# Performance work log

Hardware: AMD Instinct MI355X
Metric: run time of the kernel (lower is better)

Reference implementation:

```python
import jax, jax.numpy as jnp
import numpy as np

B, N, D = 2048, 64, 256  # batch, n_linears, n_in == n_out
N_RECURS = 3             # loop runs n_recurs + 1 = 4 times


def _make_masks():
    # per-group active block sizes in [128, 256], mimicking _init_masks
    n_act = np.minimum(128 + 32 * (np.arange(N) % 5), D)  # [N]
    col = np.arange(D)
    active = col[None, :] < n_act[:, None]                 # [N, D]
    w_mask = (active[:, :, None] & active[:, None, :]).astype(np.float32)  # [N, D, D]
    b_mask = active.astype(np.float32)                     # [N, D]
    return jnp.asarray(w_mask), jnp.asarray(b_mask)


def setup_inputs() -> dict:
    key = jax.random.key(0)
    k1, k2, k3 = jax.random.split(key, 3)
    x = jax.random.normal(k1, (B, N, D), dtype=jnp.float32)
    # kaiming_uniform-like scale for fan_in = D
    bound = 1.0 / np.sqrt(D)
    weights = jax.random.uniform(k2, (N, D, D), dtype=jnp.float32, minval=-bound, maxval=bound)
    biases = jax.random.uniform(k3, (N, D), dtype=jnp.float32, minval=-bound, maxval=bound)
    weight_mask, bias_mask = _make_masks()
    return {"x": x, "weights": weights, "biases": biases,
            "weight_mask": weight_mask, "bias_mask": bias_mask}


def reference(x, weights, biases, weight_mask, bias_mask):
    # Mask is static across recurrence steps; torch code recomputes it each
    # step but the values are identical, so hoist (same math).
    w = weights * weight_mask          # [N, D, D]
    b = (biases * bias_mask)[None]     # [1, N, D]
    for _ in range(N_RECURS + 1):
        # grouped small GEMM: x[b,n,i] @ w[n,j,i]^T -> [b,n,j]
        x = x + jax.nn.relu(jnp.einsum('bni,nji->bnj', x, w) + b)
    return x
```

## Files before the change

kernel.cpp:

```cpp
#include <hip/hip_runtime.h>
#include <hip/hip_bf16.h>
#include <cstdint>
#include <cstddef>

#define B_TOT   2048
#define N_LIN   64
#define D_DIM   256
#define NSTEPS  4
#define BT      64

typedef __attribute__((ext_vector_type(8))) short short8;
typedef __attribute__((ext_vector_type(4))) float f32x4;

__device__ __forceinline__ void split2(float f, unsigned short& h, unsigned short& l) {
    unsigned u = __float_as_uint(f);
    unsigned r = u + 0x7FFFu + ((u >> 16) & 1u);
    h = (unsigned short)(r >> 16);
    float hf = __uint_as_float(r & 0xFFFF0000u);
    float rem = f - hf;
    unsigned u2 = __float_as_uint(rem);
    unsigned r2 = u2 + 0x7FFFu + ((u2 >> 16) & 1u);
    l = (unsigned short)(r2 >> 16);
}

__device__ __forceinline__ float bf16_to_f(unsigned short s) {
    return __uint_as_float((unsigned)s << 16);
}

__global__ void prep_kernel(const float* __restrict__ w, const float* __restrict__ wm,
                            unsigned short* __restrict__ w_hi,
                            unsigned short* __restrict__ w_lo) {
    const int nW4 = N_LIN * D_DIM * D_DIM / 4;
    int stride = gridDim.x * blockDim.x;
    for (int i = blockIdx.x * blockDim.x + threadIdx.x; i < nW4; i += stride) {
        float4 wv = ((const float4*)w)[i];
        float4 mv = ((const float4*)wm)[i];
        ushort4 h, l;
        split2(wv.x * mv.x, h.x, l.x);
        split2(wv.y * mv.y, h.y, l.y);
        split2(wv.z * mv.z, h.z, l.z);
        split2(wv.w * mv.w, h.w, l.w);
        ((ushort4*)w_hi)[i] = h;
        ((ushort4*)w_lo)[i] = l;
    }
}

template <bool ONFLY>
__global__ __launch_bounds__(256, 2)
void fused_kernel(const float* __restrict__ xin,
                  const unsigned short* __restrict__ w_hi,
                  const unsigned short* __restrict__ w_lo,
                  const float* __restrict__ wraw,
                  const float* __restrict__ wmask,
                  const float* __restrict__ braw,
                  const float* __restrict__ bmask,
                  float* __restrict__ xout) {
    __shared__ unsigned short xh[BT * 256];
    __shared__ unsigned short xl[BT * 256];
    __shared__ int s_cnt[4];

    const int tid  = threadIdx.x;
    const int lane = tid & 63;
    const int wv   = tid >> 6;
    const int quad = lane >> 4;
    const int l16  = lane & 15;

    const int xcd = blockIdx.x & 7;
    const int j8  = blockIdx.x >> 3;
    const int n   = (xcd << 3) | (j8 & 7);
    const int btk = j8 >> 3;

    const size_t row_stride = (size_t)N_LIN * D_DIM;
    const float* xsrc = xin  + ((size_t)btk * BT * N_LIN + n) * D_DIM;
    float*       xdst = xout + ((size_t)btk * BT * N_LIN + n) * D_DIM;

    for (int i = tid; i < BT * (D_DIM / 4); i += 256) {
        int r = i >> 6, c4 = i & 63;
        float4 v = ((const float4*)(xsrc + (size_t)r * row_stride))[c4];
        ushort4 h, l;
        split2(v.x, h.x, l.x);
        split2(v.y, h.y, l.y);
        split2(v.z, h.z, l.z);
        split2(v.w, h.w, l.w);
        int pi = r * 256 + ((((c4 >> 1) ^ (r & 7))) << 3) + ((c4 & 1) << 2);
        *((ushort4*)&xh[pi]) = h;
        *((ushort4*)&xl[pi]) = l;
    }

    {
        float bv = bmask[n * D_DIM + wv * 64 + lane];
        unsigned long long actm = __ballot(bv != 0.0f);
        if (lane == 0) s_cnt[wv] = __popcll(actm);
    }

    float bias_r[4][4];
    #pragma unroll
    for (int jt = 0; jt < 4; ++jt)
        #pragma unroll
        for (int rg = 0; rg < 4; ++rg) {
            int c = wv * 64 + jt * 16 + quad * 4 + rg;
            bias_r[jt][rg] = braw[n * D_DIM + c] * bmask[n * D_DIM + c];
        }

    float bmj[4];
    if (ONFLY) {
        #pragma unroll
        for (int jt = 0; jt < 4; ++jt)
            bmj[jt] = bmask[n * D_DIM + wv * 64 + jt * 16 + l16];
    }

    const size_t wbase = ((size_t)n * D_DIM + (size_t)wv * 64 + l16) * D_DIM + (size_t)quad * 8;

    __syncthreads();

    const int n_act  = s_cnt[0] + s_cnt[1] + s_cnt[2] + s_cnt[3];
    const int kt_lim = n_act >> 5;
    const int c_act  = n_act - wv * 64;
    const int jt_act = (c_act <= 0) ? 0 : ((c_act >= 64) ? 4 : (c_act >> 4));

    #pragma unroll 1
    for (int step = 0; step < NSTEPS; ++step) {
        f32x4 acc[4][4];
        #pragma unroll
        for (int jt = 0; jt < 4; ++jt)
            #pragma unroll
            for (int bt = 0; bt < 4; ++bt)
                acc[jt][bt] = f32x4{0.f, 0.f, 0.f, 0.f};

        if (jt_act > 0) {
            #pragma unroll 2
            for (int kt = 0; kt < kt_lim; ++kt) {
                short8 wh[4], wl[4];
                if (!ONFLY) {
                    #pragma unroll
                    for (int jt = 0; jt < 4; ++jt) if (jt < jt_act) {
                        size_t off = wbase + (size_t)jt * 16 * D_DIM + (size_t)kt * 32;
                        wh[jt] = *((const short8*)(w_hi + off));
                        wl[jt] = *((const short8*)(w_lo + off));
                    }
                } else {
                    const float* bmi_p = bmask + n * D_DIM + kt * 32 + quad * 8;
                    float4 mi0 = ((const float4*)bmi_p)[0];
                    float4 mi1 = ((const float4*)bmi_p)[1];
                    float mi[8] = {mi0.x, mi0.y, mi0.z, mi0.w, mi1.x, mi1.y, mi1.z, mi1.w};
                    #pragma unroll
                    for (int jt = 0; jt < 4; ++jt) if (jt < jt_act) {
                        const float* wp = wraw + wbase + (size_t)jt * 16 * D_DIM + (size_t)kt * 32;
                        float4 w0 = ((const float4*)wp)[0];
                        float4 w1 = ((const float4*)wp)[1];
                        float wvv[8] = {w0.x, w0.y, w0.z, w0.w, w1.x, w1.y, w1.z, w1.w};
                        #pragma unroll
                        for (int j = 0; j < 8; ++j) {
                            unsigned short h, l;
                            split2(wvv[j] * bmj[jt] * mi[j], h, l);
                            wh[jt][j] = (short)h;
                            wl[jt][j] = (short)l;
                        }
                    }
                }
                short8 xhf[4], xlf[4];
                #pragma unroll
                for (int bt = 0; bt < 4; ++bt) {
                    int m = bt * 16 + l16;
                    int c0 = kt * 32 + quad * 8;
                    int pi = m * 256 + ((((c0 >> 3) ^ (m & 7))) << 3);
                    xhf[bt] = *((const short8*)&xh[pi]);
                    xlf[bt] = *((const short8*)&xl[pi]);
                }
                #pragma unroll
                for (int jt = 0; jt < 4; ++jt) if (jt < jt_act) {
                    #pragma unroll
                    for (int bt = 0; bt < 4; ++bt) {
                        acc[jt][bt] = __builtin_amdgcn_mfma_f32_16x16x32_bf16(wh[jt], xhf[bt], acc[jt][bt], 0, 0, 0);
                        acc[jt][bt] = __builtin_amdgcn_mfma_f32_16x16x32_bf16(wh[jt], xlf[bt], acc[jt][bt], 0, 0, 0);
                        acc[jt][bt] = __builtin_amdgcn_mfma_f32_16x16x32_bf16(wl[jt], xhf[bt], acc[jt][bt], 0, 0, 0);
                    }
                }
            }
        }

        __syncthreads();

        const bool last = (step == NSTEPS - 1);
        #pragma unroll
        for (int jt = 0; jt < 4; ++jt) {
            const bool act = (jt < jt_act);
            if (act || last) {
                #pragma unroll
                for (int bt = 0; bt < 4; ++bt) {
                    int r  = bt * 16 + l16;
                    int c0 = wv * 64 + jt * 16 + quad * 4;
                    int pi = r * 256 + ((((c0 >> 3) ^ (r & 7))) << 3) + (c0 & 7);
                    ushort4 oh = *((const ushort4*)&xh[pi]);
                    ushort4 ol = *((const ushort4*)&xl[pi]);
                    float xn[4];
                    xn[0] = bf16_to_f(oh.x) + bf16_to_f(ol.x);
                    xn[1] = bf16_to_f(oh.y) + bf16_to_f(ol.y);
                    xn[2] = bf16_to_f(oh.z) + bf16_to_f(ol.z);
                    xn[3] = bf16_to_f(oh.w) + bf16_to_f(ol.w);
                    if (act) {
                        #pragma unroll
                        for (int rg = 0; rg < 4; ++rg)
                            xn[rg] += fmaxf(acc[jt][bt][rg] + bias_r[jt][rg], 0.f);
                    }
                    if (last) {
                        float4 o;
                        o.x = xn[0]; o.y = xn[1]; o.z = xn[2]; o.w = xn[3];
                        *((float4*)(xdst + (size_t)r * row_stride + c0)) = o;
                    } else if (act) {
                        ushort4 h, l;
                        split2(xn[0], h.x, l.x);
                        split2(xn[1], h.y, l.y);
                        split2(xn[2], h.z, l.z);
                        split2(xn[3], h.w, l.w);
                        *((ushort4*)&xh[pi]) = h;
                        *((ushort4*)&xl[pi]) = l;
                    }
                }
            }
        }
        __syncthreads();
    }
}

extern "C" void kernel_launch(void* const* d_in, const int* in_sizes, int n_in,
                              void* d_out, int out_size, void* d_ws, size_t ws_size,
                              hipStream_t stream) {
    const float* x  = (const float*)d_in[0];
    const float* w  = (const float*)d_in[1];
    const float* b  = (const float*)d_in[2];
    const float* wm = (const float*)d_in[3];
    const float* bm = (const float*)d_in[4];
    float* out = (float*)d_out;

    const size_t needW = (size_t)2 * N_LIN * D_DIM * D_DIM * sizeof(unsigned short);
    const int grid = (B_TOT / BT) * N_LIN;

    if (ws_size >= needW) {
        unsigned short* w_hi = (unsigned short*)d_ws;
        unsigned short* w_lo = w_hi + (size_t)N_LIN * D_DIM * D_DIM;
        prep_kernel<<<1024, 256, 0, stream>>>(w, wm, w_hi, w_lo);
        fused_kernel<false><<<grid, 256, 0, stream>>>(x, w_hi, w_lo, w, wm, b, bm, out);
    } else {
        fused_kernel<true><<<grid, 256, 0, stream>>>(x, nullptr, nullptr, w, wm, b, bm, out);
    }
}
```

Measured before the change: 494.8 us.

## Use 8 waves per block with interleaved output-column tiles for load balance

Doubles the block to 512 threads (8 waves). Each wave now covers 16-column tiles strided by 4 across the output, instead of one contiguous 64-column block, and handles half of the 64 batch rows. The interleaving spreads the active columns of partially masked groups evenly across waves, where before some waves sat idle. The cost is that each wave loads its weight fragments with half the batch-row reuse, and the launch bound now asks for 4 blocks of 512 per CU, which limits registers per thread.

```diff
diff --git a/kernel.cpp b/kernel.cpp
--- a/kernel.cpp
+++ b/kernel.cpp
@@ -46,7 +46,7 @@
 }
 
 template <bool ONFLY>
-__global__ __launch_bounds__(256, 2)
+__global__ __launch_bounds__(512, 4)
 void fused_kernel(const float* __restrict__ xin,
                   const unsigned short* __restrict__ w_hi,
                   const unsigned short* __restrict__ w_lo,
@@ -62,6 +62,8 @@
     const int tid  = threadIdx.x;
     const int lane = tid & 63;
     const int wv   = tid >> 6;
+    const int jg   = wv & 3;
+    const int bh   = wv >> 2;
     const int quad = lane >> 4;
     const int l16  = lane & 15;
 
@@ -74,7 +76,7 @@
     const float* xsrc = xin  + ((size_t)btk * BT * N_LIN + n) * D_DIM;
     float*       xdst = xout + ((size_t)btk * BT * N_LIN + n) * D_DIM;
 
-    for (int i = tid; i < BT * (D_DIM / 4); i += 256) {
+    for (int i = tid; i < BT * (D_DIM / 4); i += 512) {
         int r = i >> 6, c4 = i & 63;
         float4 v = ((const float4*)(xsrc + (size_t)r * row_stride))[c4];
         ushort4 h, l;
@@ -87,7 +89,7 @@
         *((ushort4*)&xl[pi]) = l;
     }
 
-    {
+    if (wv < 4) {
         float bv = bmask[n * D_DIM + wv * 64 + lane];
         unsigned long long actm = __ballot(bv != 0.0f);
         if (lane == 0) s_cnt[wv] = __popcll(actm);
@@ -95,86 +97,84 @@
 
     float bias_r[4][4];
     #pragma unroll
-    for (int jt = 0; jt < 4; ++jt)
+    for (int u = 0; u < 4; ++u)
         #pragma unroll
         for (int rg = 0; rg < 4; ++rg) {
-            int c = wv * 64 + jt * 16 + quad * 4 + rg;
-            bias_r[jt][rg] = braw[n * D_DIM + c] * bmask[n * D_DIM + c];
+            int c = (jg + 4 * u) * 16 + quad * 4 + rg;
+            bias_r[u][rg] = braw[n * D_DIM + c] * bmask[n * D_DIM + c];
         }
 
     float bmj[4];
     if (ONFLY) {
         #pragma unroll
-        for (int jt = 0; jt < 4; ++jt)
-            bmj[jt] = bmask[n * D_DIM + wv * 64 + jt * 16 + l16];
-    }
-
-    const size_t wbase = ((size_t)n * D_DIM + (size_t)wv * 64 + l16) * D_DIM + (size_t)quad * 8;
+        for (int u = 0; u < 4; ++u)
+            bmj[u] = bmask[n * D_DIM + (jg + 4 * u) * 16 + l16];
+    }
+
+    const size_t wbase = ((size_t)n * D_DIM + (size_t)jg * 16 + l16) * D_DIM + (size_t)quad * 8;
 
     __syncthreads();
 
     const int n_act  = s_cnt[0] + s_cnt[1] + s_cnt[2] + s_cnt[3];
     const int kt_lim = n_act >> 5;
-    const int c_act  = n_act - wv * 64;
-    const int jt_act = (c_act <= 0) ? 0 : ((c_act >= 64) ? 4 : (c_act >> 4));
+    const int njt    = n_act >> 4;
+    const int u_cnt  = (njt - jg + 3) >> 2;
 
     #pragma unroll 1
     for (int step = 0; step < NSTEPS; ++step) {
-        f32x4 acc[4][4];
-        #pragma unroll
-        for (int jt = 0; jt < 4; ++jt)
+        f32x4 acc[4][2];
+        #pragma unroll
+        for (int u = 0; u < 4; ++u)
             #pragma unroll
-            for (int bt = 0; bt < 4; ++bt)
-                acc[jt][bt] = f32x4{0.f, 0.f, 0.f, 0.f};
-
-        if (jt_act > 0) {
-            #pragma unroll 2
-            for (int kt = 0; kt < kt_lim; ++kt) {
-                short8 wh[4], wl[4];
-                if (!ONFLY) {
+            for (int v = 0; v < 2; ++v)
+                acc[u][v] = f32x4{0.f, 0.f, 0.f, 0.f};
+
+        #pragma unroll 2
+        for (int kt = 0; kt < kt_lim; ++kt) {
+            short8 wh[4], wl[4];
+            if (!ONFLY) {
+                #pragma unroll
+                for (int u = 0; u < 4; ++u) if (u < u_cnt) {
+                    size_t off = wbase + (size_t)u * 64 * D_DIM + (size_t)kt * 32;
+                    wh[u] = *((const short8*)(w_hi + off));
+                    wl[u] = *((const short8*)(w_lo + off));
+                }
+            } else {
+                const float* bmi_p = bmask + n * D_DIM + kt * 32 + quad * 8;
+                float4 mi0 = ((const float4*)bmi_p)[0];
+                float4 mi1 = ((const float4*)bmi_p)[1];
+                float mi[8] = {mi0.x, mi0.y, mi0.z, mi0.w, mi1.x, mi1.y, mi1.z, mi1.w};
+                #pragma unroll
+                for (int u = 0; u < 4; ++u) if (u < u_cnt) {
+                    const float* wp = wraw + wbase + (size_t)u * 64 * D_DIM + (size_t)kt * 32;
+                    float4 w0 = ((const float4*)wp)[0];
+                    float4 w1 = ((const float4*)wp)[1];
+                    float wvv[8] = {w0.x, w0.y, w0.z, w0.w, w1.x, w1.y, w1.z, w1.w};
                     #pragma unroll
-                    for (int jt = 0; jt < 4; ++jt) if (jt < jt_act) {
-                        size_t off = wbase + (size_t)jt * 16 * D_DIM + (size_t)kt * 32;
-                        wh[jt] = *((const short8*)(w_hi + off));
-                        wl[jt] = *((const short8*)(w_lo + off));
+                    for (int j = 0; j < 8; ++j) {
+                        unsigned short h, l;
+                        split2(wvv[j] * bmj[u] * mi[j], h, l);
+                        wh[u][j] = (short)h;
+                        wl[u][j] = (short)l;
                     }
-                } else {
-                    const float* bmi_p = bmask + n * D_DIM + kt * 32 + quad * 8;
-                    float4 mi0 = ((const float4*)bmi_p)[0];
-                    float4 mi1 = ((const float4*)bmi_p)[1];
-                    float mi[8] = {mi0.x, mi0.y, mi0.z, mi0.w, mi1.x, mi1.y, mi1.z, mi1.w};
-                    #pragma unroll
-                    for (int jt = 0; jt < 4; ++jt) if (jt < jt_act) {
-                        const float* wp = wraw + wbase + (size_t)jt * 16 * D_DIM + (size_t)kt * 32;
-                        float4 w0 = ((const float4*)wp)[0];
-                        float4 w1 = ((const float4*)wp)[1];
-                        float wvv[8] = {w0.x, w0.y, w0.z, w0.w, w1.x, w1.y, w1.z, w1.w};
-                        #pragma unroll
-                        for (int j = 0; j < 8; ++j) {
-                            unsigned short h, l;
-                            split2(wvv[j] * bmj[jt] * mi[j], h, l);
-                            wh[jt][j] = (short)h;
-                            wl[jt][j] = (short)l;
-                        }
-                    }
-                }
-                short8 xhf[4], xlf[4];
-                #pragma unroll
-                for (int bt = 0; bt < 4; ++bt) {
-                    int m = bt * 16 + l16;
-                    int c0 = kt * 32 + quad * 8;
-                    int pi = m * 256 + ((((c0 >> 3) ^ (m & 7))) << 3);
-                    xhf[bt] = *((const short8*)&xh[pi]);
-                    xlf[bt] = *((const short8*)&xl[pi]);
-                }
-                #pragma unroll
-                for (int jt = 0; jt < 4; ++jt) if (jt < jt_act) {
-                    #pragma unroll
-                    for (int bt = 0; bt < 4; ++bt) {
-                        acc[jt][bt] = __builtin_amdgcn_mfma_f32_16x16x32_bf16(wh[jt], xhf[bt], acc[jt][bt], 0, 0, 0);
-                        acc[jt][bt] = __builtin_amdgcn_mfma_f32_16x16x32_bf16(wh[jt], xlf[bt], acc[jt][bt], 0, 0, 0);
-                        acc[jt][bt] = __builtin_amdgcn_mfma_f32_16x16x32_bf16(wl[jt], xhf[bt], acc[jt][bt], 0, 0, 0);
-                    }
+                }
+            }
+            short8 xhf[2], xlf[2];
+            #pragma unroll
+            for (int v = 0; v < 2; ++v) {
+                int m = (bh * 2 + v) * 16 + l16;
+                int c0 = kt * 32 + quad * 8;
+                int pi = m * 256 + ((((c0 >> 3) ^ (m & 7))) << 3);
+                xhf[v] = *((const short8*)&xh[pi]);
+                xlf[v] = *((const short8*)&xl[pi]);
+            }
+            #pragma unroll
+            for (int u = 0; u < 4; ++u) if (u < u_cnt) {
+                #pragma unroll
+                for (int v = 0; v < 2; ++v) {
+                    acc[u][v] = __builtin_amdgcn_mfma_f32_16x16x32_bf16(wh[u], xhf[v], acc[u][v], 0, 0, 0);
+                    acc[u][v] = __builtin_amdgcn_mfma_f32_16x16x32_bf16(wh[u], xlf[v], acc[u][v], 0, 0, 0);
+                    acc[u][v] = __builtin_amdgcn_mfma_f32_16x16x32_bf16(wl[u], xhf[v], acc[u][v], 0, 0, 0);
                 }
             }
         }
@@ -183,13 +183,13 @@
 
         const bool last = (step == NSTEPS - 1);
         #pragma unroll
-        for (int jt = 0; jt < 4; ++jt) {
-            const bool act = (jt < jt_act);
+        for (int u = 0; u < 4; ++u) {
+            const bool act = (u < u_cnt);
             if (act || last) {
                 #pragma unroll
-                for (int bt = 0; bt < 4; ++bt) {
-                    int r  = bt * 16 + l16;
-                    int c0 = wv * 64 + jt * 16 + quad * 4;
+                for (int v = 0; v < 2; ++v) {
+                    int r  = (bh * 2 + v) * 16 + l16;
+                    int c0 = (jg + 4 * u) * 16 + quad * 4;
                     int pi = r * 256 + ((((c0 >> 3) ^ (r & 7))) << 3) + (c0 & 7);
                     ushort4 oh = *((const ushort4*)&xh[pi]);
                     ushort4 ol = *((const ushort4*)&xl[pi]);
@@ -201,7 +201,7 @@
                     if (act) {
                         #pragma unroll
                         for (int rg = 0; rg < 4; ++rg)
-                            xn[rg] += fmaxf(acc[jt][bt][rg] + bias_r[jt][rg], 0.f);
+                            xn[rg] += fmaxf(acc[u][v][rg] + bias_r[u][rg], 0.f);
                     }
                     if (last) {
                         float4 o;
@@ -240,8 +240,8 @@
         unsigned short* w_hi = (unsigned short*)d_ws;
         unsigned short* w_lo = w_hi + (size_t)N_LIN * D_DIM * D_DIM;
         prep_kernel<<<1024, 256, 0, stream>>>(w, wm, w_hi, w_lo);
-        fused_kernel<false><<<grid, 256, 0, stream>>>(x, w_hi, w_lo, w, wm, b, bm, out);
+        fused_kernel<false><<<grid, 512, 0, stream>>>(x, w_hi, w_lo, w, wm, b, bm, out);
     } else {
-        fused_kernel<true><<<grid, 256, 0, stream>>>(x, nullptr, nullptr, w, wm, b, bm, out);
-    }
-}
+        fused_kernel<true><<<grid, 512, 0, stream>>>(x, nullptr, nullptr, w, wm, b, bm, out);
+    }
+}
```

New measurement: 720.4 us. +45.6%, slower.
